# Kernel optimization log

Hardware: AMD Instinct MI355X
Metric: run time of the kernel (lower is better)

The kernel has to match this reference:

```python
import jax, jax.numpy as jnp
import numpy as np

N = 100000
E = 1600000
IN_C = 128
HEADS = 4
HEAD_D = 32  # out_channels(128) // heads(4)


def setup_inputs() -> dict:
    key = jax.random.key(0)
    k1, k2, k3, k4, k5, k6 = jax.random.split(key, 6)
    x = jax.random.normal(k1, (N, IN_C), dtype=jnp.float32)
    edge_index = jax.random.randint(k2, (2, E), 0, N, dtype=jnp.int64)
    edge_weight = jax.random.uniform(k3, (E,), dtype=jnp.float32)
    # params: linear weight stored as [in, H*D] so forward is x @ W (torch does x @ weight.T)
    W = jax.random.normal(k4, (IN_C, HEADS * HEAD_D), dtype=jnp.float32) * (1.0 / np.sqrt(IN_C))
    att_src = jax.random.normal(k5, (HEADS, HEAD_D), dtype=jnp.float32) * 0.1
    att_dst = jax.random.normal(k6, (HEADS, HEAD_D), dtype=jnp.float32) * 0.1
    return {"x": x, "W": W, "att_src": att_src, "att_dst": att_dst,
            "edge_weight": edge_weight, "edge_index": edge_index, "num_nodes": N}


def reference(x, W, att_src, att_dst, edge_weight, edge_index, num_nodes):
    H, D = att_src.shape
    xw = (x @ W).reshape(-1, H, D)                       # [N, H, D]
    row, col = edge_index[0], edge_index[1]
    a_src = jnp.einsum('nhd,hd->nh', xw, att_src)        # [N, H]
    a_dst = jnp.einsum('nhd,hd->nh', xw, att_dst)        # [N, H]
    alpha = jax.nn.leaky_relu(a_src[row] + a_dst[col], negative_slope=0.2)  # [E, H]
    # segment softmax over edges grouped by row (destination of aggregation)
    amax = jax.ops.segment_max(alpha, row, num_segments=num_nodes)          # [N, H]
    amax = jnp.where(jnp.isfinite(amax), amax, 0.0)      # empty segments -> 0 (matches torch init)
    alpha = jnp.exp(alpha - amax[row])
    asum = jax.ops.segment_sum(alpha, row, num_segments=num_nodes)          # [N, H]
    alpha = alpha / (asum[row] + 1e-16)
    msg = xw[col] * alpha[..., None]                     # [E, H, D]
    out = jax.ops.segment_sum(msg, row, num_segments=num_nodes)             # [N, H, D]
    return out.reshape(num_nodes, H * D)
```

## Files before the change

### kernel.cpp

```cpp
#include <hip/hip_runtime.h>
#include <math.h>


typedef _Float16 half4 __attribute__((ext_vector_type(4)));
typedef _Float16 half8 __attribute__((ext_vector_type(8)));
typedef float    f32x4 __attribute__((ext_vector_type(4)));

#define PCHUNK   4096
#define NB_SHIFT 8
#define BCAP     4864

__device__ __forceinline__ float lrelu_exp(float v) {
    return __expf(fmaxf(v, 0.2f * v));
}

__global__ __launch_bounds__(128) void k_prep(const float* __restrict__ W,
                                              const float* __restrict__ att_src,
                                              const float* __restrict__ att_dst,
                                              _Float16* __restrict__ Wa) {
    int n = blockIdx.x;
    int k = threadIdx.x;
    float v;
    if (n < 128) {
        v = W[(size_t)k * 128 + n];
    } else if (n < 136) {
        int h = (n - 128) & 3;
        const float* att = (n < 132) ? att_src : att_dst;
        float s = 0.f;
        #pragma unroll
        for (int d = 0; d < 32; ++d)
            s += W[(size_t)k * 128 + h * 32 + d] * att[h * 32 + d];
        v = s;
    } else {
        v = 0.f;
    }
    Wa[n * 128 + k] = (_Float16)v;
}

__device__ __forceinline__ _Float16* lds_ptr(_Float16* base, int r, int kf16) {
    int g = (kf16 >> 3) ^ (r & 7);
    return base + r * 128 + g * 8 + (kf16 & 7);
}

__global__ __launch_bounds__(256) void k_gemm(const float* __restrict__ x,
                                              const _Float16* __restrict__ Wa,
                                              _Float16* __restrict__ xwh,
                                              float* __restrict__ a_src,
                                              float* __restrict__ a_dst, int N) {
    __shared__ _Float16 Xs[64 * 128];
    __shared__ _Float16 Ws[144 * 128];
    int t = threadIdx.x;
    int lane = t & 63, wv = t >> 6;
    int lm = lane & 15, lg = lane >> 4;
    int row0 = blockIdx.x * 64;

    #pragma unroll
    for (int i = 0; i < 9; ++i) {
        int f = (i * 256 + t) * 8;
        int nr = f >> 7, kc = f & 127;
        *(half8*)lds_ptr(Ws, nr, kc) = *(const half8*)&Wa[f];
    }
    #pragma unroll
    for (int i = 0; i < 4; ++i) {
        int f = (i * 256 + t) * 8;
        int r = f >> 7, kc = f & 127;
        int gr = row0 + r; if (gr >= N) gr = N - 1;
        float4 v0 = *(const float4*)&x[(size_t)gr * 128 + kc];
        float4 v1 = *(const float4*)&x[(size_t)gr * 128 + kc + 4];
        half8 hv;
        hv[0] = (_Float16)v0.x; hv[1] = (_Float16)v0.y;
        hv[2] = (_Float16)v0.z; hv[3] = (_Float16)v0.w;
        hv[4] = (_Float16)v1.x; hv[5] = (_Float16)v1.y;
        hv[6] = (_Float16)v1.z; hv[7] = (_Float16)v1.w;
        *(half8*)lds_ptr(Xs, r, kc) = hv;
    }
    __syncthreads();

    f32x4 acc[9];
    #pragma unroll
    for (int nn = 0; nn < 9; ++nn) acc[nn] = (f32x4){0.f, 0.f, 0.f, 0.f};

    #pragma unroll
    for (int kk = 0; kk < 4; ++kk) {
        int kb = kk * 32 + lg * 8;
        half8 a0 = *(const half8*)lds_ptr(Xs, wv * 16 + lm, kb);
        #pragma unroll
        for (int nn = 0; nn < 9; ++nn) {
            half8 b = *(const half8*)lds_ptr(Ws, nn * 16 + lm, kb);
            acc[nn] = __builtin_amdgcn_mfma_f32_16x16x32_f16(a0, b, acc[nn], 0, 0, 0);
        }
    }

    #pragma unroll
    for (int reg = 0; reg < 4; ++reg) {
        int row = row0 + wv * 16 + lg * 4 + reg;
        if (row < N) {
            #pragma unroll
            for (int nn = 0; nn < 8; ++nn)
                xwh[(size_t)row * 128 + nn * 16 + lm] = (_Float16)acc[nn][reg];
            float lv = acc[8][reg];
            if (lm < 4)      a_src[(size_t)row * 4 + lm]       = lv;
            else if (lm < 8) a_dst[(size_t)row * 4 + (lm - 4)] = lv;
        }
    }
}

__global__ __launch_bounds__(256) void k_part(const int* __restrict__ eidx,
                                              int* __restrict__ bctr,
                                              unsigned* __restrict__ rec,
                                              int E) {
    __shared__ unsigned long long buf[PCHUNK];
    __shared__ unsigned sbuf[PCHUNK];
    __shared__ int hist[512], excl[512], gbase[512], cur[512];
    __shared__ int wtot[4];
    int t = threadIdx.x;
    int lane = t & 63, wv = t >> 6;
    int e0 = blockIdx.x * PCHUNK;
    int nE = E - e0; if (nE > PCHUNK) nE = PCHUNK;
    hist[t] = 0; hist[t + 256] = 0;
    __syncthreads();
    for (int i = t; i < nE; i += 256) {
        int row = __builtin_nontemporal_load(&eidx[e0 + i]);
        int col = __builtin_nontemporal_load(&eidx[E + e0 + i]);
        buf[i] = ((unsigned long long)(unsigned)col << 32) | (unsigned)row;
        atomicAdd(&hist[row >> NB_SHIFT], 1);
    }
    __syncthreads();
    int h0 = hist[2 * t], h1 = hist[2 * t + 1];
    int s = h0 + h1, sc = s;
    #pragma unroll
    for (int off = 1; off < 64; off <<= 1) {
        int v = __shfl_up(sc, off);
        if (lane >= off) sc += v;
    }
    if (lane == 63) wtot[wv] = sc;
    __syncthreads();
    if (t == 0) {
        int run = 0;
        #pragma unroll
        for (int i = 0; i < 4; ++i) { int tmp = wtot[i]; wtot[i] = run; run += tmp; }
    }
    __syncthreads();
    int incl = sc + wtot[wv];
    excl[2 * t]     = incl - s;
    excl[2 * t + 1] = incl - h1;
    cur[2 * t]      = incl - s;
    cur[2 * t + 1]  = incl - h1;
    gbase[2 * t]     = h0 ? atomicAdd(&bctr[2 * t], h0) : 0;
    gbase[2 * t + 1] = h1 ? atomicAdd(&bctr[2 * t + 1], h1) : 0;
    __syncthreads();
    unsigned long long myrec[PCHUNK / 256];
    #pragma unroll
    for (int k = 0; k < PCHUNK / 256; ++k) {
        int i = t + k * 256;
        if (i < nE) myrec[k] = buf[i];
    }
    __syncthreads();
    unsigned short* bkt16 = (unsigned short*)buf;
    #pragma unroll
    for (int k = 0; k < PCHUNK / 256; ++k) {
        int i = t + k * 256;
        if (i < nE) {
            unsigned long long r = myrec[k];
            int row = (int)(unsigned)r;
            int b = row >> NB_SHIFT;
            int dst = atomicAdd(&cur[b], 1);
            sbuf[dst] = ((unsigned)(r >> 32) << 8) | ((unsigned)row & 255u);
            bkt16[dst] = (unsigned short)b;
        }
    }
    __syncthreads();
    for (int j = t; j < nE; j += 256) {
        unsigned r = sbuf[j];
        int b = bkt16[j];
        int off = gbase[b] + (j - excl[b]);
        if (off < BCAP)
            __builtin_nontemporal_store(r, &rec[(size_t)b * BCAP + off]);
    }
}

__global__ __launch_bounds__(256) void k_csr(const unsigned* __restrict__ rec,
                                             const int* __restrict__ bctr,
                                             int2* __restrict__ rseg,
                                             int* __restrict__ csr_col, int N) {
    __shared__ int cnt[256], cur[256];
    __shared__ int wtot[4];
    int b = blockIdx.x;
    int rs = b << NB_SHIFT;
    int t = threadIdx.x;
    int lane = t & 63, wv = t >> 6;
    cnt[t] = 0;
    __syncthreads();
    int m = bctr[b]; if (m > BCAP) m = BCAP;
    const unsigned* rr = &rec[(size_t)b * BCAP];
    for (int i = t; i < m; i += 256) {
        unsigned r = rr[i];
        atomicAdd(&cnt[r & 255u], 1);
    }
    __syncthreads();
    int c = cnt[t], sc = c;
    #pragma unroll
    for (int off = 1; off < 64; off <<= 1) {
        int v = __shfl_up(sc, off);
        if (lane >= off) sc += v;
    }
    if (lane == 63) wtot[wv] = sc;
    __syncthreads();
    if (t == 0) {
        int run = 0;
        #pragma unroll
        for (int i = 0; i < 4; ++i) { int tmp = wtot[i]; wtot[i] = run; run += tmp; }
    }
    __syncthreads();
    int ex = sc + wtot[wv] - c;
    cur[t] = ex;
    int n = rs + t;
    if (n < N) {
        int2 sg;
        sg.x = b * BCAP + ex;
        sg.y = b * BCAP + ex + c;
        rseg[n] = sg;
    }
    __syncthreads();
    for (int i = t; i < m; i += 256) {
        unsigned r = rr[i];
        int slot = atomicAdd(&cur[r & 255u], 1);
        csr_col[b * BCAP + slot] = (int)(r >> 8);
    }
}

__global__ __launch_bounds__(256) void k_agg(const int2* __restrict__ rseg,
                                             const int* __restrict__ csr_col,
                                             const float* __restrict__ a_src,
                                             const float* __restrict__ a_dst,
                                             const _Float16* __restrict__ xwh,
                                             float* __restrict__ out,
                                             int n0, int n1) {
    int lane = threadIdx.x & 63;
    int n = n0 + blockIdx.x * 4 + (threadIdx.x >> 6);
    if (n >= n1) return;
    int2 seg = rseg[n];
    int beg = seg.x, end = seg.y;
    int q = lane >> 4;
    int l = lane & 15;
    int h = l >> 2;
    float s_n = a_src[(size_t)n * 4 + h];
    float acc[8] = {0, 0, 0, 0, 0, 0, 0, 0};
    float ws = 0.f;

    for (int w0 = beg; w0 < end; w0 += 64) {
        int rem = end - w0; if (rem > 64) rem = 64;
        int cc = (lane < rem) ? __builtin_nontemporal_load(&csr_col[w0 + lane]) : 0;
        int j = 0;
        for (; j + 16 <= rem; j += 16) {
            int c[4]; float ad[4]; half8 xv[4];
            #pragma unroll
            for (int u = 0; u < 4; ++u) c[u] = __shfl(cc, j + u * 4 + q);
            #pragma unroll
            for (int u = 0; u < 4; ++u) {
                ad[u] = a_dst[(size_t)c[u] * 4 + h];
                xv[u] = *(const half8*)&xwh[(size_t)c[u] * 128 + (l << 3)];
            }
            #pragma unroll
            for (int u = 0; u < 4; ++u) {
                float w = lrelu_exp(s_n + ad[u]);
                ws += w;
                #pragma unroll
                for (int k = 0; k < 8; ++k)
                    acc[k] += w * (float)xv[u][k];
            }
        }
        if (j < rem) {
            int c[4]; float m[4]; float ad[4]; half8 xv[4];
            #pragma unroll
            for (int u = 0; u < 4; ++u) {
                int r = j + u * 4 + q;
                c[u] = __shfl(cc, r);
                m[u] = (r < rem) ? 1.f : 0.f;
            }
            #pragma unroll
            for (int u = 0; u < 4; ++u) {
                ad[u] = a_dst[(size_t)c[u] * 4 + h];
                xv[u] = *(const half8*)&xwh[(size_t)c[u] * 128 + (l << 3)];
            }
            #pragma unroll
            for (int u = 0; u < 4; ++u) {
                float w = m[u] * lrelu_exp(s_n + ad[u]);
                ws += w;
                #pragma unroll
                for (int k = 0; k < 8; ++k)
                    acc[k] += w * (float)xv[u][k];
            }
        }
    }

    #pragma unroll
    for (int k = 0; k < 8; ++k) {
        acc[k] += __shfl_xor(acc[k], 16);
        acc[k] += __shfl_xor(acc[k], 32);
    }
    ws += __shfl_xor(ws, 16);
    ws += __shfl_xor(ws, 32);
    if (q == 0) {
        float inv = 1.0f / (ws + 1e-16f);
        f32x4 o0 = {acc[0] * inv, acc[1] * inv, acc[2] * inv, acc[3] * inv};
        f32x4 o1 = {acc[4] * inv, acc[5] * inv, acc[6] * inv, acc[7] * inv};
        __builtin_nontemporal_store(o0, (f32x4*)&out[(size_t)n * 128 + (l << 3)]);
        __builtin_nontemporal_store(o1, (f32x4*)&out[(size_t)n * 128 + (l << 3) + 4]);
    }
}

extern "C" void kernel_launch(void* const* d_in, const int* in_sizes, int n_in,
                              void* d_out, int out_size, void* d_ws, size_t ws_size,
                              hipStream_t stream) {
    const float* x       = (const float*)d_in[0];
    const float* W       = (const float*)d_in[1];
    const float* att_src = (const float*)d_in[2];
    const float* att_dst = (const float*)d_in[3];
    const int* eidx      = (const int*)d_in[5];
    int N = in_sizes[0] / 128;
    int E = in_sizes[4];
    float* out = (float*)d_out;

    char* p = (char*)d_ws;
    auto alloc = [&](size_t bytes) {
        char* r = p;
        p += (bytes + 255) & ~(size_t)255;
        return r;
    };
    int nbuckets = (N + 255) >> NB_SHIFT;
    _Float16* xwh  = (_Float16*)alloc((size_t)N * 128 * 2);
    float* a_src   = (float*)alloc((size_t)N * 4 * 4);
    float* a_dst   = (float*)alloc((size_t)N * 4 * 4);
    int*   bctr    = (int*)  alloc(512 * 4);
    unsigned* rec  = (unsigned*)alloc((size_t)nbuckets * BCAP * 4);
    int2*  rseg    = (int2*) alloc((size_t)N * 8);
    int*   csr_col = (int*)  alloc((size_t)nbuckets * BCAP * 4);
    _Float16* Wa   = (_Float16*)alloc(144 * 128 * 2);

    (void)hipMemsetAsync(bctr, 0, 512 * 4, stream);
    k_prep<<<144, 128, 0, stream>>>(W, att_src, att_dst, Wa);
    k_gemm<<<(N + 63) / 64, 256, 0, stream>>>(x, Wa, xwh, a_src, a_dst, N);
    k_part<<<(E + PCHUNK - 1) / PCHUNK, 256, 0, stream>>>(eidx, bctr, rec, E);
    k_csr<<<nbuckets, 256, 0, stream>>>(rec, bctr, rseg, csr_col, N);
    int half = N / 2;
    k_agg<<<(half + 3) / 4, 256, 0, stream>>>(rseg, csr_col, a_src, a_dst, xwh, out, 0, half);
    k_agg<<<(N - half + 3) / 4, 256, 0, stream>>>(rseg, csr_col, a_src, a_dst, xwh, out, half, N);
}
```

Before: 240.1 us.

## Fuse GEMM and edge partition into one interleaved kernel; widen CSR blocks

Merges the feature GEMM and the edge bucketing pass into a single launch. Partition blocks are interleaved at a fixed stride among GEMM blocks and share one raw shared-memory buffer, so the two independent stages can run concurrently and fill the GPU together. The CSR build kernel moves from 256 to 1024 threads per block to spread each bucket's edges over more threads. In exchange, every block reserves the larger shared-memory footprint, which may reduce GEMM occupancy, and the block-to-role index mapping becomes more intricate.

```diff
diff --git a/kernel.cpp b/kernel.cpp
--- a/kernel.cpp
+++ b/kernel.cpp
@@ -42,17 +42,100 @@
     return base + r * 128 + g * 8 + (kf16 & 7);
 }
 
-__global__ __launch_bounds__(256) void k_gemm(const float* __restrict__ x,
-                                              const _Float16* __restrict__ Wa,
-                                              _Float16* __restrict__ xwh,
-                                              float* __restrict__ a_src,
-                                              float* __restrict__ a_dst, int N) {
-    __shared__ _Float16 Xs[64 * 128];
-    __shared__ _Float16 Ws[144 * 128];
+__global__ __launch_bounds__(256) void k_fat(const float* __restrict__ x,
+                                             const _Float16* __restrict__ Wa,
+                                             _Float16* __restrict__ xwh,
+                                             float* __restrict__ a_src,
+                                             float* __restrict__ a_dst, int N,
+                                             const int* __restrict__ eidx,
+                                             int* __restrict__ bctr,
+                                             unsigned* __restrict__ rec, int E,
+                                             int nPart, int stride) {
+    __shared__ __align__(16) char smem[57360];
+    int bid = blockIdx.x;
     int t = threadIdx.x;
     int lane = t & 63, wv = t >> 6;
+    int q = bid / stride, r = bid - q * stride;
+
+    if (r == 0 && q < nPart) {
+        unsigned long long* buf = (unsigned long long*)smem;
+        unsigned* sbuf = (unsigned*)(smem + 32768);
+        int* hist = (int*)(smem + 49152);
+        int* excl = hist + 512;
+        int* gbase = excl + 512;
+        int* cur = gbase + 512;
+        int* wtot = cur + 512;
+        int e0 = q * PCHUNK;
+        int nE = E - e0; if (nE > PCHUNK) nE = PCHUNK;
+        hist[t] = 0; hist[t + 256] = 0;
+        __syncthreads();
+        for (int i = t; i < nE; i += 256) {
+            int row = __builtin_nontemporal_load(&eidx[e0 + i]);
+            int col = __builtin_nontemporal_load(&eidx[E + e0 + i]);
+            buf[i] = ((unsigned long long)(unsigned)col << 32) | (unsigned)row;
+            atomicAdd(&hist[row >> NB_SHIFT], 1);
+        }
+        __syncthreads();
+        int h0 = hist[2 * t], h1 = hist[2 * t + 1];
+        int s = h0 + h1, sc = s;
+        #pragma unroll
+        for (int off = 1; off < 64; off <<= 1) {
+            int v = __shfl_up(sc, off);
+            if (lane >= off) sc += v;
+        }
+        if (lane == 63) wtot[wv] = sc;
+        __syncthreads();
+        if (t == 0) {
+            int run = 0;
+            #pragma unroll
+            for (int i = 0; i < 4; ++i) { int tmp = wtot[i]; wtot[i] = run; run += tmp; }
+        }
+        __syncthreads();
+        int incl = sc + wtot[wv];
+        excl[2 * t]     = incl - s;
+        excl[2 * t + 1] = incl - h1;
+        cur[2 * t]      = incl - s;
+        cur[2 * t + 1]  = incl - h1;
+        gbase[2 * t]     = h0 ? atomicAdd(&bctr[2 * t], h0) : 0;
+        gbase[2 * t + 1] = h1 ? atomicAdd(&bctr[2 * t + 1], h1) : 0;
+        __syncthreads();
+        unsigned long long myrec[PCHUNK / 256];
+        #pragma unroll
+        for (int k = 0; k < PCHUNK / 256; ++k) {
+            int i = t + k * 256;
+            if (i < nE) myrec[k] = buf[i];
+        }
+        __syncthreads();
+        unsigned short* bkt16 = (unsigned short*)buf;
+        #pragma unroll
+        for (int k = 0; k < PCHUNK / 256; ++k) {
+            int i = t + k * 256;
+            if (i < nE) {
+                unsigned long long rr = myrec[k];
+                int row = (int)(unsigned)rr;
+                int b = row >> NB_SHIFT;
+                int dst = atomicAdd(&cur[b], 1);
+                sbuf[dst] = ((unsigned)(rr >> 32) << 8) | ((unsigned)row & 255u);
+                bkt16[dst] = (unsigned short)b;
+            }
+        }
+        __syncthreads();
+        for (int j = t; j < nE; j += 256) {
+            unsigned rr = sbuf[j];
+            int b = bkt16[j];
+            int off = gbase[b] + (j - excl[b]);
+            if (off < BCAP)
+                __builtin_nontemporal_store(rr, &rec[(size_t)b * BCAP + off]);
+        }
+        return;
+    }
+
+    int nb = q + (r ? 1 : 0); if (nb > nPart) nb = nPart;
+    int gid = bid - nb;
+    _Float16* Xs = (_Float16*)smem;
+    _Float16* Ws = (_Float16*)(smem + 16384);
     int lm = lane & 15, lg = lane >> 4;
-    int row0 = blockIdx.x * 64;
+    int row0 = gid * 64;
 
     #pragma unroll
     for (int i = 0; i < 9; ++i) {
@@ -63,8 +146,8 @@
     #pragma unroll
     for (int i = 0; i < 4; ++i) {
         int f = (i * 256 + t) * 8;
-        int r = f >> 7, kc = f & 127;
-        int gr = row0 + r; if (gr >= N) gr = N - 1;
+        int rr = f >> 7, kc = f & 127;
+        int gr = row0 + rr; if (gr >= N) gr = N - 1;
         float4 v0 = *(const float4*)&x[(size_t)gr * 128 + kc];
         float4 v1 = *(const float4*)&x[(size_t)gr * 128 + kc + 4];
         half8 hv;
@@ -72,7 +155,7 @@
         hv[2] = (_Float16)v0.z; hv[3] = (_Float16)v0.w;
         hv[4] = (_Float16)v1.x; hv[5] = (_Float16)v1.y;
         hv[6] = (_Float16)v1.z; hv[7] = (_Float16)v1.w;
-        *(half8*)lds_ptr(Xs, r, kc) = hv;
+        *(half8*)lds_ptr(Xs, rr, kc) = hv;
     }
     __syncthreads();
 
@@ -105,106 +188,33 @@
     }
 }
 
-__global__ __launch_bounds__(256) void k_part(const int* __restrict__ eidx,
-                                              int* __restrict__ bctr,
-                                              unsigned* __restrict__ rec,
-                                              int E) {
-    __shared__ unsigned long long buf[PCHUNK];
-    __shared__ unsigned sbuf[PCHUNK];
-    __shared__ int hist[512], excl[512], gbase[512], cur[512];
-    __shared__ int wtot[4];
-    int t = threadIdx.x;
-    int lane = t & 63, wv = t >> 6;
-    int e0 = blockIdx.x * PCHUNK;
-    int nE = E - e0; if (nE > PCHUNK) nE = PCHUNK;
-    hist[t] = 0; hist[t + 256] = 0;
-    __syncthreads();
-    for (int i = t; i < nE; i += 256) {
-        int row = __builtin_nontemporal_load(&eidx[e0 + i]);
-        int col = __builtin_nontemporal_load(&eidx[E + e0 + i]);
-        buf[i] = ((unsigned long long)(unsigned)col << 32) | (unsigned)row;
-        atomicAdd(&hist[row >> NB_SHIFT], 1);
-    }
-    __syncthreads();
-    int h0 = hist[2 * t], h1 = hist[2 * t + 1];
-    int s = h0 + h1, sc = s;
-    #pragma unroll
-    for (int off = 1; off < 64; off <<= 1) {
-        int v = __shfl_up(sc, off);
-        if (lane >= off) sc += v;
-    }
-    if (lane == 63) wtot[wv] = sc;
-    __syncthreads();
-    if (t == 0) {
-        int run = 0;
-        #pragma unroll
-        for (int i = 0; i < 4; ++i) { int tmp = wtot[i]; wtot[i] = run; run += tmp; }
-    }
-    __syncthreads();
-    int incl = sc + wtot[wv];
-    excl[2 * t]     = incl - s;
-    excl[2 * t + 1] = incl - h1;
-    cur[2 * t]      = incl - s;
-    cur[2 * t + 1]  = incl - h1;
-    gbase[2 * t]     = h0 ? atomicAdd(&bctr[2 * t], h0) : 0;
-    gbase[2 * t + 1] = h1 ? atomicAdd(&bctr[2 * t + 1], h1) : 0;
-    __syncthreads();
-    unsigned long long myrec[PCHUNK / 256];
-    #pragma unroll
-    for (int k = 0; k < PCHUNK / 256; ++k) {
-        int i = t + k * 256;
-        if (i < nE) myrec[k] = buf[i];
-    }
-    __syncthreads();
-    unsigned short* bkt16 = (unsigned short*)buf;
-    #pragma unroll
-    for (int k = 0; k < PCHUNK / 256; ++k) {
-        int i = t + k * 256;
-        if (i < nE) {
-            unsigned long long r = myrec[k];
-            int row = (int)(unsigned)r;
-            int b = row >> NB_SHIFT;
-            int dst = atomicAdd(&cur[b], 1);
-            sbuf[dst] = ((unsigned)(r >> 32) << 8) | ((unsigned)row & 255u);
-            bkt16[dst] = (unsigned short)b;
-        }
-    }
-    __syncthreads();
-    for (int j = t; j < nE; j += 256) {
-        unsigned r = sbuf[j];
-        int b = bkt16[j];
-        int off = gbase[b] + (j - excl[b]);
-        if (off < BCAP)
-            __builtin_nontemporal_store(r, &rec[(size_t)b * BCAP + off]);
-    }
-}
-
-__global__ __launch_bounds__(256) void k_csr(const unsigned* __restrict__ rec,
-                                             const int* __restrict__ bctr,
-                                             int2* __restrict__ rseg,
-                                             int* __restrict__ csr_col, int N) {
+__global__ __launch_bounds__(1024) void k_csr(const unsigned* __restrict__ rec,
+                                              const int* __restrict__ bctr,
+                                              int2* __restrict__ rseg,
+                                              int* __restrict__ csr_col, int N) {
     __shared__ int cnt[256], cur[256];
     __shared__ int wtot[4];
     int b = blockIdx.x;
     int rs = b << NB_SHIFT;
     int t = threadIdx.x;
     int lane = t & 63, wv = t >> 6;
-    cnt[t] = 0;
+    if (t < 256) cnt[t] = 0;
     __syncthreads();
     int m = bctr[b]; if (m > BCAP) m = BCAP;
     const unsigned* rr = &rec[(size_t)b * BCAP];
-    for (int i = t; i < m; i += 256) {
+    for (int i = t; i < m; i += 1024) {
         unsigned r = rr[i];
         atomicAdd(&cnt[r & 255u], 1);
     }
     __syncthreads();
-    int c = cnt[t], sc = c;
+    int c = (t < 256) ? cnt[t] : 0;
+    int sc = c;
     #pragma unroll
     for (int off = 1; off < 64; off <<= 1) {
         int v = __shfl_up(sc, off);
         if (lane >= off) sc += v;
     }
-    if (lane == 63) wtot[wv] = sc;
+    if (t < 256 && lane == 63) wtot[wv] = sc;
     __syncthreads();
     if (t == 0) {
         int run = 0;
@@ -212,17 +222,19 @@
         for (int i = 0; i < 4; ++i) { int tmp = wtot[i]; wtot[i] = run; run += tmp; }
     }
     __syncthreads();
-    int ex = sc + wtot[wv] - c;
-    cur[t] = ex;
-    int n = rs + t;
-    if (n < N) {
-        int2 sg;
-        sg.x = b * BCAP + ex;
-        sg.y = b * BCAP + ex + c;
-        rseg[n] = sg;
-    }
-    __syncthreads();
-    for (int i = t; i < m; i += 256) {
+    if (t < 256) {
+        int ex = sc + wtot[wv] - c;
+        cur[t] = ex;
+        int n = rs + t;
+        if (n < N) {
+            int2 sg;
+            sg.x = b * BCAP + ex;
+            sg.y = b * BCAP + ex + c;
+            rseg[n] = sg;
+        }
+    }
+    __syncthreads();
+    for (int i = t; i < m; i += 1024) {
         unsigned r = rr[i];
         int slot = atomicAdd(&cur[r & 255u], 1);
         csr_col[b * BCAP + slot] = (int)(r >> 8);
@@ -338,11 +350,16 @@
     int*   csr_col = (int*)  alloc((size_t)nbuckets * BCAP * 4);
     _Float16* Wa   = (_Float16*)alloc(144 * 128 * 2);
 
+    int nPart = (E + PCHUNK - 1) / PCHUNK;
+    int nGemm = (N + 63) / 64;
+    int total = nPart + nGemm;
+    int stride = total / nPart; if (stride < 1) stride = 1;
+
     (void)hipMemsetAsync(bctr, 0, 512 * 4, stream);
     k_prep<<<144, 128, 0, stream>>>(W, att_src, att_dst, Wa);
-    k_gemm<<<(N + 63) / 64, 256, 0, stream>>>(x, Wa, xwh, a_src, a_dst, N);
-    k_part<<<(E + PCHUNK - 1) / PCHUNK, 256, 0, stream>>>(eidx, bctr, rec, E);
-    k_csr<<<nbuckets, 256, 0, stream>>>(rec, bctr, rseg, csr_col, N);
+    k_fat<<<total, 256, 0, stream>>>(x, Wa, xwh, a_src, a_dst, N,
+                                     eidx, bctr, rec, E, nPart, stride);
+    k_csr<<<nbuckets, 1024, 0, stream>>>(rec, bctr, rseg, csr_col, N);
     int half = N / 2;
     k_agg<<<(half + 3) / 4, 256, 0, stream>>>(rseg, csr_col, a_src, a_dst, xwh, out, 0, half);
     k_agg<<<(N - half + 3) / 4, 256, 0, stream>>>(rseg, csr_col, a_src, a_dst, xwh, out, half, N);
```

New measurement: 251.4 us. 1.05x slower.
